# Kernel tuning notes

Hardware: AMD Instinct MI355X
Metric: run time of the kernel (lower is better)

## Reference

```python
import jax, jax.numpy as jnp
import numpy as np


def setup_inputs() -> dict:
    key = jax.random.key(0)
    ks = jax.random.split(key, 5)
    B, C, H, W = 4, 256, 64, 64
    Cq = C // 8
    x = jax.random.normal(ks[0], (B, C, H, W), dtype=jnp.float32)
    Wq = jax.random.normal(ks[1], (Cq, C), dtype=jnp.float32) * (1.0 / np.sqrt(C))
    Wk = jax.random.normal(ks[2], (Cq, C), dtype=jnp.float32) * (1.0 / np.sqrt(C))
    Wv = jax.random.normal(ks[3], (C, C), dtype=jnp.float32) * (1.0 / np.sqrt(C))
    bq = jnp.zeros((Cq,), dtype=jnp.float32)
    bk = jnp.zeros((Cq,), dtype=jnp.float32)
    bv = jnp.zeros((C,), dtype=jnp.float32)
    gamma = jnp.ones((1,), dtype=jnp.float32)
    return {"x": x, "Wq": Wq, "bq": bq, "Wk": Wk, "bk": bk, "Wv": Wv, "bv": bv, "gamma": gamma}


def reference(x, Wq, bq, Wk, bk, Wv, bv, gamma):
    B, C, H, W = x.shape
    N = H * W
    xf = x.reshape(B, C, N)                      # (B, C, N)
    # 1x1 convs == per-pixel linear projections over channels
    q = jnp.einsum('dc,bcn->bdn', Wq, xf) + bq[None, :, None]   # (B, C/8, N)
    k = jnp.einsum('dc,bcn->bdn', Wk, xf) + bk[None, :, None]   # (B, C/8, N)
    v = jnp.einsum('dc,bcn->bdn', Wv, xf) + bv[None, :, None]   # (B, C,   N)
    # attention: note original has NO 1/sqrt(d) scaling
    scores = jnp.einsum('bdn,bdm->bnm', q, k)     # (B, N, N)
    attn = jax.nn.softmax(scores, axis=-1)
    out = jnp.einsum('bnm,bdm->bnd', attn, v)     # (B, N, C)
    out = out.transpose(0, 2, 1).reshape(B, C, H, W)
    return gamma * out + x
```

## Files before the change

### kernel.cpp

```cpp
#include <hip/hip_runtime.h>

#define BATCH 4
#define CH    256
#define DQ    32
#define NPIX  4096
#define LOG2E 1.4426950408889634f

typedef unsigned short u16;
typedef unsigned int   u32;
typedef __attribute__((ext_vector_type(8))) short short8;
typedef __attribute__((ext_vector_type(16))) float f32x16;

#if defined(__has_builtin)
#if __has_builtin(__builtin_amdgcn_exp2f)
#define EXP2F(x) __builtin_amdgcn_exp2f(x)
#else
#define EXP2F(x) __expf((x) * 0.6931471805599453f)
#endif
#else
#define EXP2F(x) __expf((x) * 0.6931471805599453f)
#endif

__device__ __forceinline__ float b2f(u32 u) {
  union { u32 i; float f; } v; v.i = (u & 0xffffu) << 16; return v.f;
}
__device__ __forceinline__ u16 f2b(float f) {
  union { float f; u32 i; } v; v.f = f;
  u32 x = v.i; x += 0x7fffu + ((x >> 16) & 1u);
  return (u16)(x >> 16);
}
__device__ __forceinline__ u32 pack_hi16(float lo, float hi) {
  union { float f; u32 i; } a, b; a.f = lo; b.f = hi;
  return __builtin_amdgcn_perm(b.i, a.i, 0x07060302u);
}

__global__ __launch_bounds__(256) void wconv(
    const float* __restrict__ Wq, const float* __restrict__ Wk,
    const float* __restrict__ Wv, u16* __restrict__ wsz, u16* __restrict__ wsz_lo)
{
  const int blk = blockIdx.x;
  const int jt = blk >> 4, kk = blk & 15;
  #pragma unroll
  for (int rep = 0; rep < 2; ++rep) {
    const int idx = rep * 256 + threadIdx.x;
    const int j = idx >> 4, el = idx & 15, e = kk * 16 + el;
    const float* Wsrc = (jt == 0) ? Wq : (jt == 1) ? Wk : Wv;
    const int row = (jt <= 1) ? j : (jt - 2) * 32 + j;
    float v = Wsrc[(size_t)row * CH + e];
    if (jt == 0) v *= LOG2E;
    const u16 hi = f2b(v);
    const int o = (((jt * 16 + kk) * 2 + (el >> 3)) * 32 + j) * 8 + (el & 7);
    wsz[o] = hi;
    if (jt < 2) wsz_lo[o] = f2b(v - b2f(hi));
  }
}

__global__ __launch_bounds__(256) void proj(
    const float* __restrict__ x,
    const u16* __restrict__ wsz, const u16* __restrict__ wsz_lo,
    const float* __restrict__ bq, const float* __restrict__ bk, const float* __restrict__ bv,
    u16* __restrict__ q_t, u16* __restrict__ k_t, u16* __restrict__ v_swz)
{
  const int nt = blockIdx.x, b = blockIdx.y;
  const int n0 = nt * 32;
  const int t = threadIdx.x;
  const int w = t >> 6, hl = (t >> 5) & 1, l31 = t & 31;

  __shared__ __align__(16) u16 xh[32 * 264];
  __shared__ __align__(16) u16 xl[32 * 264];

  #pragma unroll
  for (int p = 0; p < 8; ++p) {
    const int e = p * 32 + (t >> 3), n4 = (t & 7) * 4;
    const float4 v4 = *(const float4*)&x[((size_t)b * CH + e) * NPIX + n0 + n4];
    const float vv[4] = {v4.x, v4.y, v4.z, v4.w};
    #pragma unroll
    for (int jj = 0; jj < 4; ++jj) {
      const u16 hi = f2b(vv[jj]);
      xh[(n4 + jj) * 264 + e] = hi;
      xl[(n4 + jj) * 264 + e] = f2b(vv[jj] - b2f(hi));
    }
  }
  __syncthreads();

  const int n = n0 + l31;

  if (w <= 1) {
    const int jt = w;
    f32x16 a0, a1, a2;
    #pragma unroll
    for (int r = 0; r < 16; ++r) { a0[r] = 0.f; a1[r] = 0.f; a2[r] = 0.f; }
    #pragma unroll
    for (int kk = 0; kk < 16; ++kk) {
      const int wo = ((jt * 16 + kk) * 2 + hl) * 256 + l31 * 8;
      const short8 Ah = *(const short8*)&wsz[wo];
      const short8 Al = *(const short8*)&wsz_lo[wo];
      const int xo = l31 * 264 + kk * 16 + hl * 8;
      const short8 Bh = *(const short8*)&xh[xo];
      const short8 Bl = *(const short8*)&xl[xo];
      a0 = __builtin_amdgcn_mfma_f32_32x32x16_bf16(Ah, Bh, a0, 0, 0, 0);
      a1 = __builtin_amdgcn_mfma_f32_32x32x16_bf16(Ah, Bl, a1, 0, 0, 0);
      a2 = __builtin_amdgcn_mfma_f32_32x32x16_bf16(Al, Bh, a2, 0, 0, 0);
    }
    u16* dst = (jt == 0) ? q_t : k_t;
    const float* bias = (jt == 0) ? bq : bk;
    const float bscale = (jt == 0) ? LOG2E : 1.0f;
    #pragma unroll
    for (int r = 0; r < 16; ++r) {
      const int d = (r & 3) + 8 * (r >> 2) + 4 * hl;
      dst[((size_t)b * NPIX + n) * DQ + d] =
        f2b((a0[r] + a1[r]) + (a2[r] + bias[d] * bscale));
    }
  } else {
    #pragma unroll
    for (int ci = 0; ci < 4; ++ci) {
      const int ctv = (w - 2) * 4 + ci;
      const int jt = 2 + ctv;
      f32x16 a0, a1;
      #pragma unroll
      for (int r = 0; r < 16; ++r) { a0[r] = 0.f; a1[r] = 0.f; }
      #pragma unroll
      for (int kk = 0; kk < 16; kk += 2) {
        const short8 Ah0 = *(const short8*)&wsz[((jt * 16 + kk) * 2 + hl) * 256 + l31 * 8];
        const short8 Bh0 = *(const short8*)&xh[l31 * 264 + kk * 16 + hl * 8];
        const short8 Ah1 = *(const short8*)&wsz[((jt * 16 + kk + 1) * 2 + hl) * 256 + l31 * 8];
        const short8 Bh1 = *(const short8*)&xh[l31 * 264 + (kk + 1) * 16 + hl * 8];
        a0 = __builtin_amdgcn_mfma_f32_32x32x16_bf16(Ah0, Bh0, a0, 0, 0, 0);
        a1 = __builtin_amdgcn_mfma_f32_32x32x16_bf16(Ah1, Bh1, a1, 0, 0, 0);
      }
      const int kc = (l31 >> 4) & 1, h3 = (l31 >> 3) & 1, j8 = l31 & 7;
      u16* dst = v_swz + (((((size_t)b * 128 + nt) * 8 + ctv) * 2 + kc) * 2 + h3) * 256 + j8;
      #pragma unroll
      for (int r = 0; r < 16; ++r) {
        const int c5 = (r & 3) + 8 * (r >> 2) + 4 * hl;
        dst[c5 * 8] = f2b(a0[r] + a1[r] + bv[ctv * 32 + c5]);
      }
    }
  }
}

__global__ __launch_bounds__(512, 1) void attn(
    const u16* __restrict__ q_t, const u16* __restrict__ k_t,
    const u16* __restrict__ v_swz, const float* __restrict__ x,
    const float* __restrict__ gamma, float* __restrict__ out)
{
  const int b = blockIdx.y, t = threadIdx.x;
  const int w = t >> 6, lane = t & 63, hl = lane >> 5, l31 = lane & 31;
  const int mq = w >> 1, ch = w & 1;
  const int n0 = blockIdx.x * 64;

  __shared__ float cbuf[16384];
  __shared__ float lbuf[8][2][64];

  short8 qf[2][2];
  #pragma unroll
  for (int nt = 0; nt < 2; ++nt)
    #pragma unroll
    for (int kd = 0; kd < 2; ++kd)
      qf[nt][kd] = *(const short8*)(q_t + ((size_t)b * NPIX + n0 + nt * 32 + l31) * DQ + kd * 16 + hl * 8);

  f32x16 acc[8];
  #pragma unroll
  for (int a = 0; a < 8; ++a)
    #pragma unroll
    for (int r = 0; r < 16; ++r) acc[a][r] = 0.f;
  float lrun[2] = {0.f, 0.f};

  const u16* kb = k_t + (size_t)b * NPIX * DQ;
  const u16* vb = v_swz + (size_t)b * 128 * 8192;

  for (int cc = 0; cc < 32; ++cc) {
    const int mc = mq * 32 + cc;

    const u16* kp = kb + (size_t)(mc * 32 + l31) * DQ + hl * 8;
    const short8 kf0 = *(const short8*)(kp);
    const short8 kf1 = *(const short8*)(kp + 16);

    const u16* vp = vb + (size_t)mc * 8192 + (size_t)hl * 256 + l31 * 8;
    short8 av[4];
    #pragma unroll
    for (int ct = 0; ct < 4; ++ct)
      av[ct] = *(const short8*)(vp + (((ch * 4 + ct) * 2 + 0) * 2) * 256);

    union { uint4 u; short8 s; } bu[2][2];
    #pragma unroll
    for (int nt = 0; nt < 2; ++nt) {
      f32x16 st;
      #pragma unroll
      for (int r = 0; r < 16; ++r) st[r] = 0.f;
      st = __builtin_amdgcn_mfma_f32_32x32x16_bf16(kf0, qf[nt][0], st, 0, 0, 0);
      st = __builtin_amdgcn_mfma_f32_32x32x16_bf16(kf1, qf[nt][1], st, 0, 0, 0);
      u32 pk[4][2];
      #pragma unroll
      for (int g = 0; g < 4; ++g) {
        const float e0 = EXP2F(st[4 * g + 0]);
        const float e1 = EXP2F(st[4 * g + 1]);
        const float e2 = EXP2F(st[4 * g + 2]);
        const float e3 = EXP2F(st[4 * g + 3]);
        lrun[nt] += (e0 + e1) + (e2 + e3);
        pk[g][0] = pack_hi16(e0, e1);
        pk[g][1] = pack_hi16(e2, e3);
      }
      #pragma unroll
      for (int kc = 0; kc < 2; ++kc) {
        const u32 s0 = hl ? pk[2 * kc][0] : pk[2 * kc + 1][0];
        const u32 s1 = hl ? pk[2 * kc][1] : pk[2 * kc + 1][1];
        const u32 r0 = (u32)__shfl_xor((int)s0, 32);
        const u32 r1 = (u32)__shfl_xor((int)s1, 32);
        bu[nt][kc].u.x = hl ? r0 : pk[2 * kc][0];
        bu[nt][kc].u.y = hl ? r1 : pk[2 * kc][1];
        bu[nt][kc].u.z = hl ? pk[2 * kc + 1][0] : r0;
        bu[nt][kc].u.w = hl ? pk[2 * kc + 1][1] : r1;
      }
    }

    #pragma unroll
    for (int ct = 0; ct < 4; ++ct)
      #pragma unroll
      for (int nt = 0; nt < 2; ++nt)
        acc[nt * 4 + ct] =
          __builtin_amdgcn_mfma_f32_32x32x16_bf16(av[ct], bu[nt][0].s, acc[nt * 4 + ct], 0, 0, 0);

    #pragma unroll
    for (int ct = 0; ct < 4; ++ct)
      av[ct] = *(const short8*)(vp + (((ch * 4 + ct) * 2 + 1) * 2) * 256);
    #pragma unroll
    for (int ct = 0; ct < 4; ++ct)
      #pragma unroll
      for (int nt = 0; nt < 2; ++nt)
        acc[nt * 4 + ct] =
          __builtin_amdgcn_mfma_f32_32x32x16_bf16(av[ct], bu[nt][1].s, acc[nt * 4 + ct], 0, 0, 0);
  }

  lbuf[w][0][lane] = lrun[0];
  lbuf[w][1][lane] = lrun[1];

  #pragma unroll
  for (int nt = 0; nt < 2; ++nt) {
    if (mq == 1 || mq == 3) {
      const int slot = (ch * 2 + (mq >> 1)) * 4096;
      #pragma unroll
      for (int ct = 0; ct < 4; ++ct)
        #pragma unroll
        for (int r = 0; r < 16; ++r)
          cbuf[slot + (ct * 16 + r) * 64 + lane] = acc[nt * 4 + ct][r];
    }
    __syncthreads();
    if (mq == 0 || mq == 2) {
      const int slot = (ch * 2 + (mq >> 1)) * 4096;
      #pragma unroll
      for (int ct = 0; ct < 4; ++ct)
        #pragma unroll
        for (int r = 0; r < 16; ++r)
          acc[nt * 4 + ct][r] += cbuf[slot + (ct * 16 + r) * 64 + lane];
    }
    __syncthreads();
    if (mq == 2) {
      const int slot = ch * 2 * 4096;
      #pragma unroll
      for (int ct = 0; ct < 4; ++ct)
        #pragma unroll
        for (int r = 0; r < 16; ++r)
          cbuf[slot + (ct * 16 + r) * 64 + lane] = acc[nt * 4 + ct][r];
    }
    __syncthreads();
    if (mq == 0) {
      const int slot = ch * 2 * 4096;
      #pragma unroll
      for (int ct = 0; ct < 4; ++ct)
        #pragma unroll
        for (int r = 0; r < 16; ++r)
          acc[nt * 4 + ct][r] += cbuf[slot + (ct * 16 + r) * 64 + lane];
    }
    __syncthreads();
  }

  if (mq == 0) {
    const float g = gamma[0];
    #pragma unroll
    for (int nt = 0; nt < 2; ++nt) {
      float l = 0.f;
      #pragma unroll
      for (int ww = 0; ww < 8; ++ww) l += lbuf[ww][nt][lane];
      l += __shfl_xor(l, 32);
      const float linv = 2.0f / l;
      #pragma unroll
      for (int ct = 0; ct < 4; ++ct)
        #pragma unroll
        for (int r = 0; r < 16; ++r) {
          const int c = (ch * 4 + ct) * 32 + (r & 3) + 8 * (r >> 2) + 4 * hl;
          const size_t idx = ((size_t)b * CH + c) * NPIX + n0 + nt * 32 + l31;
          out[idx] = g * acc[nt * 4 + ct][r] * linv + x[idx];
        }
    }
  }
}

extern "C" void kernel_launch(void* const* d_in, const int* in_sizes, int n_in,
                              void* d_out, int out_size, void* d_ws, size_t ws_size,
                              hipStream_t stream) {
  const float* x  = (const float*)d_in[0];
  const float* Wq = (const float*)d_in[1];
  const float* bq = (const float*)d_in[2];
  const float* Wk = (const float*)d_in[3];
  const float* bk = (const float*)d_in[4];
  const float* Wv = (const float*)d_in[5];
  const float* bv = (const float*)d_in[6];
  const float* gm = (const float*)d_in[7];
  float* out = (float*)d_out;

  const size_t qk_e = (size_t)BATCH * NPIX * DQ;
  const size_t v_e  = (size_t)BATCH * NPIX * CH;
  const size_t w_e  = 10 * 16 * 2 * 32 * 8;
  const size_t wl_e = 2 * 16 * 2 * 32 * 8;
  const size_t need = (2 * qk_e + v_e + w_e + wl_e) * sizeof(u16);
  if (ws_size < need) return;

  u16* q_t    = (u16*)d_ws;
  u16* k_t    = q_t + qk_e;
  u16* v_swz  = k_t + qk_e;
  u16* wsz    = v_swz + v_e;
  u16* wsz_lo = wsz + w_e;

  wconv<<<dim3(160), 256, 0, stream>>>(Wq, Wk, Wv, wsz, wsz_lo);
  proj <<<dim3(NPIX / 32, BATCH), 256, 0, stream>>>(x, wsz, wsz_lo, bq, bk, bv, q_t, k_t, v_swz);
  attn <<<dim3(NPIX / 64, BATCH), 512, 0, stream>>>(q_t, k_t, v_swz, x, gm, out);
}
```

Measured before the change: 188.6 us.

## Restructure attention kernel: LDS-staged V double buffer, shared P tiles, no split-K reduction

The attention kernel stops splitting the key dimension across waves. Each wave now owns one 32-pixel query tile and a quarter of the channels and walks all 128 key chunks. V chunks are staged into LDS with asynchronous global_load_lds double buffering. The softmax probability tiles are computed once by two waves per query tile and shared through LDS, which removes the cross-wave LDS reduction of accumulators and cuts register pressure (2 accumulators instead of 8). The block index is also remapped for batch/tile locality and the occupancy hint is relaxed. The cost is one __syncthreads per key chunk and serialised P computation by a subset of waves.

```diff
diff --git a/kernel.cpp b/kernel.cpp
--- a/kernel.cpp
+++ b/kernel.cpp
@@ -139,159 +139,147 @@
   }
 }
 
-__global__ __launch_bounds__(512, 1) void attn(
+struct PHalf { u32 p00, p01, p10, p11; };
+
+template <int H>
+__device__ __forceinline__ void compute_p_half(
+    const short8 kf0, const short8 kf1, const short8 qf0, const short8 qf1,
+    const int hl, const int lane, float& lrun, u16* __restrict__ pdst)
+{
+  f32x16 st;
+  #pragma unroll
+  for (int r = 0; r < 16; ++r) st[r] = 0.f;
+  st = __builtin_amdgcn_mfma_f32_32x32x16_bf16(kf0, qf0, st, 0, 0, 0);
+  st = __builtin_amdgcn_mfma_f32_32x32x16_bf16(kf1, qf1, st, 0, 0, 0);
+  const float e0 = EXP2F(st[8 * H + 0]);
+  const float e1 = EXP2F(st[8 * H + 1]);
+  const float e2 = EXP2F(st[8 * H + 2]);
+  const float e3 = EXP2F(st[8 * H + 3]);
+  const float e4 = EXP2F(st[8 * H + 4]);
+  const float e5 = EXP2F(st[8 * H + 5]);
+  const float e6 = EXP2F(st[8 * H + 6]);
+  const float e7 = EXP2F(st[8 * H + 7]);
+  lrun += ((e0 + e1) + (e2 + e3)) + ((e4 + e5) + (e6 + e7));
+  const u32 p00 = pack_hi16(e0, e1), p01 = pack_hi16(e2, e3);
+  const u32 p10 = pack_hi16(e4, e5), p11 = pack_hi16(e6, e7);
+  const u32 s0 = hl ? p00 : p10;
+  const u32 s1 = hl ? p01 : p11;
+  const u32 r0 = (u32)__shfl_xor((int)s0, 32);
+  const u32 r1 = (u32)__shfl_xor((int)s1, 32);
+  uint4 bu;
+  bu.x = hl ? r0 : p00;
+  bu.y = hl ? r1 : p01;
+  bu.z = hl ? p10 : r0;
+  bu.w = hl ? p11 : r1;
+  *(uint4*)(pdst + lane * 8) = bu;
+}
+
+__global__ __launch_bounds__(512) void attn(
     const u16* __restrict__ q_t, const u16* __restrict__ k_t,
     const u16* __restrict__ v_swz, const float* __restrict__ x,
     const float* __restrict__ gamma, float* __restrict__ out)
 {
-  const int b = blockIdx.y, t = threadIdx.x;
+  const int blk = blockIdx.x;
+  const int b = (blk & 7) >> 1;
+  const int tile = ((blk >> 3) << 1) | (blk & 1);
+  const int n0 = tile * 64;
+  const int t = threadIdx.x;
   const int w = t >> 6, lane = t & 63, hl = lane >> 5, l31 = lane & 31;
-  const int mq = w >> 1, ch = w & 1;
-  const int n0 = blockIdx.x * 64;
-
-  __shared__ float cbuf[16384];
-  __shared__ float lbuf[8][2][64];
-
-  short8 qf[2][2];
-  #pragma unroll
-  for (int nt = 0; nt < 2; ++nt)
-    #pragma unroll
-    for (int kd = 0; kd < 2; ++kd)
-      qf[nt][kd] = *(const short8*)(q_t + ((size_t)b * NPIX + n0 + nt * 32 + l31) * DQ + kd * 16 + hl * 8);
-
-  f32x16 acc[8];
-  #pragma unroll
-  for (int a = 0; a < 8; ++a)
+  const int nt = w >> 2, ch = w & 3;
+  const int dch = ch - nt;
+  const int hrole = (dch == 0) ? 0 : (dch == 2) ? 1 : -1;
+
+  __shared__ __align__(16) u16 vlds[2][8192];
+  __shared__ __align__(16) u16 plds[2][2][2][512];
+  __shared__ float lbufs[2][2][32];
+
+  const u16* kb = k_t + (size_t)b * NPIX * DQ;
+  const u16* vbase = v_swz + (size_t)b * 128 * 8192;
+
+  short8 qf0{}, qf1{};
+  if (hrole >= 0) {
+    const u16* qp = q_t + ((size_t)b * NPIX + n0 + nt * 32 + l31) * DQ + hl * 8;
+    qf0 = *(const short8*)(qp);
+    qf1 = *(const short8*)(qp + 16);
+  }
+
+  f32x16 acc[2];
+  #pragma unroll
+  for (int a = 0; a < 2; ++a)
     #pragma unroll
     for (int r = 0; r < 16; ++r) acc[a][r] = 0.f;
-  float lrun[2] = {0.f, 0.f};
-
-  const u16* kb = k_t + (size_t)b * NPIX * DQ;
-  const u16* vb = v_swz + (size_t)b * 128 * 8192;
-
-  for (int cc = 0; cc < 32; ++cc) {
-    const int mc = mq * 32 + cc;
-
-    const u16* kp = kb + (size_t)(mc * 32 + l31) * DQ + hl * 8;
+  float lrun = 0.f;
+
+  auto stageV = [&](int mc, int buf) {
+    const u16* src = vbase + (size_t)mc * 8192;
+    #pragma unroll
+    for (int s = 0; s < 2; ++s) {
+      const int off = (w * 2 + s) * 512 + lane * 8;
+      __builtin_amdgcn_global_load_lds(
+          (const __attribute__((address_space(1))) void*)(src + off),
+          (__attribute__((address_space(3))) void*)(&vlds[buf][off]), 16, 0, 0);
+    }
+  };
+
+  stageV(0, 0);
+  if (hrole >= 0) {
+    const u16* kp = kb + (size_t)l31 * DQ + hl * 8;
     const short8 kf0 = *(const short8*)(kp);
     const short8 kf1 = *(const short8*)(kp + 16);
-
-    const u16* vp = vb + (size_t)mc * 8192 + (size_t)hl * 256 + l31 * 8;
-    short8 av[4];
-    #pragma unroll
-    for (int ct = 0; ct < 4; ++ct)
-      av[ct] = *(const short8*)(vp + (((ch * 4 + ct) * 2 + 0) * 2) * 256);
-
-    union { uint4 u; short8 s; } bu[2][2];
-    #pragma unroll
-    for (int nt = 0; nt < 2; ++nt) {
-      f32x16 st;
-      #pragma unroll
-      for (int r = 0; r < 16; ++r) st[r] = 0.f;
-      st = __builtin_amdgcn_mfma_f32_32x32x16_bf16(kf0, qf[nt][0], st, 0, 0, 0);
-      st = __builtin_amdgcn_mfma_f32_32x32x16_bf16(kf1, qf[nt][1], st, 0, 0, 0);
-      u32 pk[4][2];
-      #pragma unroll
-      for (int g = 0; g < 4; ++g) {
-        const float e0 = EXP2F(st[4 * g + 0]);
-        const float e1 = EXP2F(st[4 * g + 1]);
-        const float e2 = EXP2F(st[4 * g + 2]);
-        const float e3 = EXP2F(st[4 * g + 3]);
-        lrun[nt] += (e0 + e1) + (e2 + e3);
-        pk[g][0] = pack_hi16(e0, e1);
-        pk[g][1] = pack_hi16(e2, e3);
+    if (hrole == 0) compute_p_half<0>(kf0, kf1, qf0, qf1, hl, lane, lrun, &plds[0][nt][0][0]);
+    else            compute_p_half<1>(kf0, kf1, qf0, qf1, hl, lane, lrun, &plds[0][nt][1][0]);
+  }
+  __syncthreads();
+
+  for (int cc = 0; cc < 128; ++cc) {
+    const int buf = cc & 1;
+    short8 kf0{}, kf1{};
+    if (cc < 127) {
+      stageV(cc + 1, buf ^ 1);
+      if (hrole >= 0) {
+        const u16* kp = kb + (size_t)((cc + 1) * 32 + l31) * DQ + hl * 8;
+        kf0 = *(const short8*)(kp);
+        kf1 = *(const short8*)(kp + 16);
       }
+    }
+
+    union { uint4 u; short8 s; } pf[2];
+    pf[0].u = *(const uint4*)&plds[buf][nt][0][lane * 8];
+    pf[1].u = *(const uint4*)&plds[buf][nt][1][lane * 8];
+    #pragma unroll
+    for (int ct2 = 0; ct2 < 2; ++ct2) {
+      const int ct = ch * 2 + ct2;
       #pragma unroll
       for (int kc = 0; kc < 2; ++kc) {
-        const u32 s0 = hl ? pk[2 * kc][0] : pk[2 * kc + 1][0];
-        const u32 s1 = hl ? pk[2 * kc][1] : pk[2 * kc + 1][1];
-        const u32 r0 = (u32)__shfl_xor((int)s0, 32);
-        const u32 r1 = (u32)__shfl_xor((int)s1, 32);
-        bu[nt][kc].u.x = hl ? r0 : pk[2 * kc][0];
-        bu[nt][kc].u.y = hl ? r1 : pk[2 * kc][1];
-        bu[nt][kc].u.z = hl ? pk[2 * kc + 1][0] : r0;
-        bu[nt][kc].u.w = hl ? pk[2 * kc + 1][1] : r1;
+        const short8 av = *(const short8*)&vlds[buf][((ct * 2 + kc) * 2 + hl) * 256 + l31 * 8];
+        acc[ct2] = __builtin_amdgcn_mfma_f32_32x32x16_bf16(av, pf[kc].s, acc[ct2], 0, 0, 0);
       }
     }
 
-    #pragma unroll
-    for (int ct = 0; ct < 4; ++ct)
-      #pragma unroll
-      for (int nt = 0; nt < 2; ++nt)
-        acc[nt * 4 + ct] =
-          __builtin_amdgcn_mfma_f32_32x32x16_bf16(av[ct], bu[nt][0].s, acc[nt * 4 + ct], 0, 0, 0);
-
-    #pragma unroll
-    for (int ct = 0; ct < 4; ++ct)
-      av[ct] = *(const short8*)(vp + (((ch * 4 + ct) * 2 + 1) * 2) * 256);
-    #pragma unroll
-    for (int ct = 0; ct < 4; ++ct)
-      #pragma unroll
-      for (int nt = 0; nt < 2; ++nt)
-        acc[nt * 4 + ct] =
-          __builtin_amdgcn_mfma_f32_32x32x16_bf16(av[ct], bu[nt][1].s, acc[nt * 4 + ct], 0, 0, 0);
-  }
-
-  lbuf[w][0][lane] = lrun[0];
-  lbuf[w][1][lane] = lrun[1];
-
-  #pragma unroll
-  for (int nt = 0; nt < 2; ++nt) {
-    if (mq == 1 || mq == 3) {
-      const int slot = (ch * 2 + (mq >> 1)) * 4096;
-      #pragma unroll
-      for (int ct = 0; ct < 4; ++ct)
-        #pragma unroll
-        for (int r = 0; r < 16; ++r)
-          cbuf[slot + (ct * 16 + r) * 64 + lane] = acc[nt * 4 + ct][r];
+    if (cc < 127 && hrole >= 0) {
+      if (hrole == 0) compute_p_half<0>(kf0, kf1, qf0, qf1, hl, lane, lrun, &plds[buf ^ 1][nt][0][0]);
+      else            compute_p_half<1>(kf0, kf1, qf0, qf1, hl, lane, lrun, &plds[buf ^ 1][nt][1][0]);
     }
     __syncthreads();
-    if (mq == 0 || mq == 2) {
-      const int slot = (ch * 2 + (mq >> 1)) * 4096;
-      #pragma unroll
-      for (int ct = 0; ct < 4; ++ct)
-        #pragma unroll
-        for (int r = 0; r < 16; ++r)
-          acc[nt * 4 + ct][r] += cbuf[slot + (ct * 16 + r) * 64 + lane];
-    }
-    __syncthreads();
-    if (mq == 2) {
-      const int slot = ch * 2 * 4096;
-      #pragma unroll
-      for (int ct = 0; ct < 4; ++ct)
-        #pragma unroll
-        for (int r = 0; r < 16; ++r)
-          cbuf[slot + (ct * 16 + r) * 64 + lane] = acc[nt * 4 + ct][r];
-    }
-    __syncthreads();
-    if (mq == 0) {
-      const int slot = ch * 2 * 4096;
-      #pragma unroll
-      for (int ct = 0; ct < 4; ++ct)
-        #pragma unroll
-        for (int r = 0; r < 16; ++r)
-          acc[nt * 4 + ct][r] += cbuf[slot + (ct * 16 + r) * 64 + lane];
-    }
-    __syncthreads();
-  }
-
-  if (mq == 0) {
-    const float g = gamma[0];
-    #pragma unroll
-    for (int nt = 0; nt < 2; ++nt) {
-      float l = 0.f;
-      #pragma unroll
-      for (int ww = 0; ww < 8; ++ww) l += lbuf[ww][nt][lane];
-      l += __shfl_xor(l, 32);
-      const float linv = 2.0f / l;
-      #pragma unroll
-      for (int ct = 0; ct < 4; ++ct)
-        #pragma unroll
-        for (int r = 0; r < 16; ++r) {
-          const int c = (ch * 4 + ct) * 32 + (r & 3) + 8 * (r >> 2) + 4 * hl;
-          const size_t idx = ((size_t)b * CH + c) * NPIX + n0 + nt * 32 + l31;
-          out[idx] = g * acc[nt * 4 + ct][r] * linv + x[idx];
-        }
+  }
+
+  if (hrole >= 0) {
+    const float ls = lrun + __shfl_xor(lrun, 32);
+    if (hl == 0) lbufs[nt][hrole][l31] = ls;
+  }
+  __syncthreads();
+
+  const float l = lbufs[nt][0][l31] + lbufs[nt][1][l31];
+  const float linv = 1.0f / l;
+  const float g = gamma[0];
+  #pragma unroll
+  for (int ct2 = 0; ct2 < 2; ++ct2) {
+    const int ct = ch * 2 + ct2;
+    #pragma unroll
+    for (int r = 0; r < 16; ++r) {
+      const int c = ct * 32 + (r & 3) + 8 * (r >> 2) + 4 * hl;
+      const size_t idx = ((size_t)b * CH + c) * NPIX + n0 + nt * 32 + l31;
+      out[idx] = g * acc[ct2][r] * linv + x[idx];
     }
   }
 }
@@ -324,5 +312,5 @@
 
   wconv<<<dim3(160), 256, 0, stream>>>(Wq, Wk, Wv, wsz, wsz_lo);
   proj <<<dim3(NPIX / 32, BATCH), 256, 0, stream>>>(x, wsz, wsz_lo, bq, bk, bv, q_t, k_t, v_swz);
-  attn <<<dim3(NPIX / 64, BATCH), 512, 0, stream>>>(q_t, k_t, v_swz, x, gm, out);
-}
+  attn <<<dim3(256), 512, 0, stream>>>(q_t, k_t, v_swz, x, gm, out);
+}
```

Result: slower. 220.5 us (+16.9%).
